# Kernel tuning notes

Hardware: AMD Instinct MI355X
Metric: run time of the kernel (lower is better)

## Reference

```python
import jax, jax.numpy as jnp
import numpy as np
from itertools import combinations

NUM_FIELDS = 40
EMB_DIM = 64
BATCH = 2048
PAIRS = NUM_FIELDS * (NUM_FIELDS - 1) // 2  # 780

def _triu_indices():
    idx = np.array(list(combinations(range(NUM_FIELDS), 2)), dtype=np.int32)  # [PAIRS, 2]
    return idx[:, 0], idx[:, 1]

def setup_inputs() -> dict:
    key = jax.random.key(0)
    k1, k2 = jax.random.split(key)
    feature_emb = jax.random.normal(k1, (BATCH, NUM_FIELDS, EMB_DIM), dtype=jnp.float32)
    # xavier_normal for [PAIRS, EMB_DIM, EMB_DIM]: fan_in = fan_out = EMB_DIM
    std = float(np.sqrt(2.0 / (EMB_DIM + EMB_DIM)))
    bilinear_W = jax.random.normal(k2, (PAIRS, EMB_DIM, EMB_DIM), dtype=jnp.float32) * std
    left_idx, right_idx = _triu_indices()
    return {
        "feature_emb": feature_emb,
        "bilinear_W": bilinear_W,
        "left_idx": jnp.asarray(left_idx),
        "right_idx": jnp.asarray(right_idx),
    }

def reference(feature_emb, bilinear_W, left_idx, right_idx):
    # field_interaction: per-pair bilinear form
    left_emb = feature_emb[:, left_idx]    # [B, PAIRS, D]
    right_emb = feature_emb[:, right_idx]  # [B, PAIRS, D]
    # (left @ W_p) * right, per pair p
    out = jnp.einsum('bpd,pde->bpe', left_emb, bilinear_W) * right_emb
    return out
```

## Files before the change

### kernel.cpp

```cpp
#include <hip/hip_runtime.h>

#define BATCH   2048
#define NFIELDS 40
#define EMB     64
#define PAIRS   780
#define BM      128
#define NTILES  (BATCH / BM)
#define NBLOCKS (PAIRS * NTILES)
#define FEMB_ELEMS (BATCH * NFIELDS * EMB)
#define W_ELEMS    (PAIRS * EMB * EMB)

typedef __attribute__((ext_vector_type(8))) short          short8;
typedef __attribute__((ext_vector_type(8))) unsigned short ushort8;
typedef __attribute__((ext_vector_type(4))) float          fvec4;

__device__ __forceinline__ unsigned short f2bf(float f) {
    unsigned int x = __float_as_uint(f);
    return (unsigned short)((x + 0x7fffu + ((x >> 16) & 1u)) >> 16);
}
__device__ __forceinline__ float bf2f(unsigned short h) {
    return __uint_as_float(((unsigned int)h) << 16);
}
struct bfpair { unsigned short h, l; };
__device__ __forceinline__ bfpair split1(float f) {
    bfpair r;
    r.h = f2bf(f);
    r.l = f2bf(f - bf2f(r.h));
    return r;
}

__global__ __launch_bounds__(256) void prep_femb(
    const float* __restrict__ femb, unsigned short* __restrict__ Fh,
    unsigned short* __restrict__ Fl)
{
    int tid  = blockIdx.x * 256 + threadIdx.x;
    int base = tid * 8;
    fvec4 a = *(const fvec4*)&femb[base];
    fvec4 b = *(const fvec4*)&femb[base + 4];
    ushort8 hi, lo;
    #pragma unroll
    for (int i = 0; i < 4; ++i) {
        bfpair s0 = split1(a[i]);
        hi[i] = s0.h; lo[i] = s0.l;
        bfpair s1 = split1(b[i]);
        hi[i + 4] = s1.h; lo[i + 4] = s1.l;
    }
    *(ushort8*)&Fh[base] = hi;
    *(ushort8*)&Fl[base] = lo;
}

__global__ __launch_bounds__(256) void prep_w(
    const float* __restrict__ W, unsigned short* __restrict__ Wh,
    unsigned short* __restrict__ Wl)
{
    __shared__ float Ws[EMB * EMB];
    int p = blockIdx.x;
    int t = threadIdx.x;
    const float* Wp = W + (size_t)p * (EMB * EMB);
    #pragma unroll
    for (int j = 0; j < 4; ++j)
        *(fvec4*)&Ws[t * 16 + j * 4] = *(const fvec4*)&Wp[t * 16 + j * 4];
    __syncthreads();

    int e  = t & 63;
    int k0 = (t >> 6) * 16;
    #pragma unroll
    for (int j = 0; j < 2; ++j) {
        int k = k0 + j * 8;
        ushort8 hi, lo;
        #pragma unroll
        for (int i = 0; i < 8; ++i) {
            bfpair s = split1(Ws[(k + i) * EMB + e]);
            hi[i] = s.h; lo[i] = s.l;
        }
        size_t dst = (size_t)p * (EMB * EMB) + e * EMB + k;
        *(ushort8*)&Wh[dst] = hi;
        *(ushort8*)&Wl[dst] = lo;
    }
}

__global__ __launch_bounds__(256, 4) void bilinear_main(
    const unsigned short* __restrict__ Fh, const unsigned short* __restrict__ Fl,
    const unsigned short* __restrict__ Wh, const unsigned short* __restrict__ Wl,
    const float* __restrict__ femb,
    const int* __restrict__ lidx, const int* __restrict__ ridx,
    float* __restrict__ out)
{
    int d  = blockIdx.x;
    int w  = (d & 7) * (NBLOCKS / 8) + (d >> 3);
    int p  = w >> 4;
    int b0 = (w & 15) * BM;

    int lp = lidx[p];
    int rp = ridx[p];
    int t  = threadIdx.x;
    int wv = t >> 6;
    int l  = t & 63;
    int r  = l & 15;
    int g  = l >> 4;

    const unsigned short* WhP = Wh + (size_t)p * (EMB * EMB);
    const unsigned short* WlP = Wl + (size_t)p * (EMB * EMB);

    fvec4 acc[2][4] = {};
    #pragma unroll
    for (int kk = 0; kk < 2; ++kk) {
        short8 Ah[4], Al[4], Bh[2], Bl[2];
        #pragma unroll
        for (int n = 0; n < 4; ++n) {
            int off = (n * 16 + r) * EMB + kk * 32 + g * 8;
            Ah[n] = *(const short8*)&WhP[off];
            Al[n] = *(const short8*)&WlP[off];
        }
        #pragma unroll
        for (int m = 0; m < 2; ++m) {
            size_t off = ((size_t)(b0 + wv * 32 + m * 16 + r) * NFIELDS + lp) * EMB
                       + kk * 32 + g * 8;
            Bh[m] = *(const short8*)&Fh[off];
            Bl[m] = *(const short8*)&Fl[off];
        }
        #pragma unroll
        for (int m = 0; m < 2; ++m)
            #pragma unroll
            for (int n = 0; n < 4; ++n) {
                acc[m][n] = __builtin_amdgcn_mfma_f32_16x16x32_bf16(Al[n], Bh[m], acc[m][n], 0, 0, 0);
                acc[m][n] = __builtin_amdgcn_mfma_f32_16x16x32_bf16(Ah[n], Bl[m], acc[m][n], 0, 0, 0);
                acc[m][n] = __builtin_amdgcn_mfma_f32_16x16x32_bf16(Ah[n], Bh[m], acc[m][n], 0, 0, 0);
            }
    }

    #pragma unroll
    for (int m = 0; m < 2; ++m) {
        int b = b0 + wv * 32 + m * 16 + r;
        const float* Rr = femb + ((size_t)b * NFIELDS + rp) * EMB;
        float*       Or = out  + ((size_t)b * PAIRS   + p)  * EMB;
        #pragma unroll
        for (int n = 0; n < 4; ++n) {
            int e0 = n * 16 + g * 4;
            fvec4 rv = *(const fvec4*)&Rr[e0];
            fvec4 o  = acc[m][n] * rv;
            *(fvec4*)&Or[e0] = o;
        }
    }
}

extern "C" void kernel_launch(void* const* d_in, const int* in_sizes, int n_in,
                              void* d_out, int out_size, void* d_ws, size_t ws_size,
                              hipStream_t stream) {
    const float* femb = (const float*)d_in[0];
    const float* W    = (const float*)d_in[1];
    const int*   lidx = (const int*)d_in[2];
    const int*   ridx = (const int*)d_in[3];
    float*       out  = (float*)d_out;

    unsigned short* Fh  = (unsigned short*)d_ws;
    unsigned short* Fl  = Fh + FEMB_ELEMS;
    unsigned short* Whg = Fl + FEMB_ELEMS;
    unsigned short* Wlg = Whg + W_ELEMS;

    prep_femb<<<FEMB_ELEMS / (256 * 8), 256, 0, stream>>>(femb, Fh, Fl);
    prep_w   <<<PAIRS, 256, 0, stream>>>(W, Whg, Wlg);
    bilinear_main<<<NBLOCKS, 256, 0, stream>>>(Fh, Fl, Whg, Wlg, femb, lidx, ridx, out);
}
```

Baseline: 591.0 us.

## Pre-pack bf16 operands into MFMA fragment layout and swap operand roles

Both prep kernels now write the hi/lo bf16 splits of the embeddings and weights directly in per-lane MFMA fragment order. The main kernel can then load each fragment with one contiguous 16-byte-per-lane access instead of strided row reads. The embedding and weight operands swap roles in the MFMA, so each lane now holds four consecutive batch rows for one output column. As a result the epilogue changes from float4 stores to scalar loads and stores. This removes scattered operand loads, but it multiplies the number of store and load instructions on the dominant output write stream.

```diff
diff --git a/kernel.cpp b/kernel.cpp
--- a/kernel.cpp
+++ b/kernel.cpp
@@ -29,24 +29,38 @@
     return r;
 }
 
+
 __global__ __launch_bounds__(256) void prep_femb(
     const float* __restrict__ femb, unsigned short* __restrict__ Fh,
     unsigned short* __restrict__ Fl)
 {
-    int tid  = blockIdx.x * 256 + threadIdx.x;
-    int base = tid * 8;
-    fvec4 a = *(const fvec4*)&femb[base];
-    fvec4 b = *(const fvec4*)&femb[base + 4];
-    ushort8 hi, lo;
+    int tid = blockIdx.x * 256 + threadIdx.x;
+    int r   = tid & 15;
+    int bf  = tid >> 4;
+    int f   = bf % NFIELDS;
+    int b4  = bf / NFIELDS;
+
+    const float* src = femb + ((size_t)(b4 * 16 + r) * NFIELDS + f) * EMB;
+    ushort8 h8[8], l8[8];
     #pragma unroll
-    for (int i = 0; i < 4; ++i) {
-        bfpair s0 = split1(a[i]);
-        hi[i] = s0.h; lo[i] = s0.l;
-        bfpair s1 = split1(b[i]);
-        hi[i + 4] = s1.h; lo[i + 4] = s1.l;
+    for (int c = 0; c < 8; ++c) {
+        fvec4 a = *(const fvec4*)&src[c * 8];
+        fvec4 b = *(const fvec4*)&src[c * 8 + 4];
+        #pragma unroll
+        for (int i = 0; i < 4; ++i) {
+            bfpair s0 = split1(a[i]); h8[c][i]     = s0.h; l8[c][i]     = s0.l;
+            bfpair s1 = split1(b[i]); h8[c][i + 4] = s1.h; l8[c][i + 4] = s1.l;
+        }
     }
-    *(ushort8*)&Fh[base] = hi;
-    *(ushort8*)&Fl[base] = lo;
+    #pragma unroll
+    for (int kk = 0; kk < 2; ++kk)
+        #pragma unroll
+        for (int g = 0; g < 4; ++g) {
+            int c = kk * 4 + g;
+            size_t dst = ((((size_t)bf * 2) + kk) * 64 + g * 16 + r) * 8;
+            *(ushort8*)&Fh[dst] = h8[c];
+            *(ushort8*)&Fl[dst] = l8[c];
+        }
 }
 
 __global__ __launch_bounds__(256) void prep_w(
@@ -62,18 +76,21 @@
         *(fvec4*)&Ws[t * 16 + j * 4] = *(const fvec4*)&Wp[t * 16 + j * 4];
     __syncthreads();
 
-    int e  = t & 63;
-    int k0 = (t >> 6) * 16;
     #pragma unroll
-    for (int j = 0; j < 2; ++j) {
-        int k = k0 + j * 8;
+    for (int half = 0; half < 2; ++half) {
+        int c  = t + half * 256;
+        int kk = c >> 8;
+        int n  = (c >> 6) & 3;
+        int l  = c & 63;
+        int r  = l & 15;
+        int g  = l >> 4;
         ushort8 hi, lo;
         #pragma unroll
         for (int i = 0; i < 8; ++i) {
-            bfpair s = split1(Ws[(k + i) * EMB + e]);
+            bfpair s = split1(Ws[(kk * 32 + g * 8 + i) * EMB + n * 16 + r]);
             hi[i] = s.h; lo[i] = s.l;
         }
-        size_t dst = (size_t)p * (EMB * EMB) + e * EMB + k;
+        size_t dst = (size_t)p * 4096 + (size_t)c * 8;
         *(ushort8*)&Wh[dst] = hi;
         *(ushort8*)&Wl[dst] = lo;
     }
@@ -89,7 +106,7 @@
     int d  = blockIdx.x;
     int w  = (d & 7) * (NBLOCKS / 8) + (d >> 3);
     int p  = w >> 4;
-    int b0 = (w & 15) * BM;
+    int bt = w & 15;
 
     int lp = lidx[p];
     int rp = ridx[p];
@@ -99,47 +116,47 @@
     int r  = l & 15;
     int g  = l >> 4;
 
-    const unsigned short* WhP = Wh + (size_t)p * (EMB * EMB);
-    const unsigned short* WlP = Wl + (size_t)p * (EMB * EMB);
-
     fvec4 acc[2][4] = {};
     #pragma unroll
     for (int kk = 0; kk < 2; ++kk) {
-        short8 Ah[4], Al[4], Bh[2], Bl[2];
+        short8 Bh[4], Bl[4];
         #pragma unroll
         for (int n = 0; n < 4; ++n) {
-            int off = (n * 16 + r) * EMB + kk * 32 + g * 8;
-            Ah[n] = *(const short8*)&WhP[off];
-            Al[n] = *(const short8*)&WlP[off];
+            size_t off = ((size_t)p * 8 + kk * 4 + n) * 512 + l * 8;
+            Bh[n] = *(const short8*)&Wh[off];
+            Bl[n] = *(const short8*)&Wl[off];
         }
+        short8 Ah[2], Al[2];
         #pragma unroll
         for (int m = 0; m < 2; ++m) {
-            size_t off = ((size_t)(b0 + wv * 32 + m * 16 + r) * NFIELDS + lp) * EMB
-                       + kk * 32 + g * 8;
-            Bh[m] = *(const short8*)&Fh[off];
-            Bl[m] = *(const short8*)&Fl[off];
+            int b4a = bt * 8 + wv * 2 + m;
+            size_t off = (((size_t)b4a * NFIELDS + lp) * 2 + kk) * 512 + l * 8;
+            Ah[m] = *(const short8*)&Fh[off];
+            Al[m] = *(const short8*)&Fl[off];
         }
         #pragma unroll
         for (int m = 0; m < 2; ++m)
             #pragma unroll
             for (int n = 0; n < 4; ++n) {
-                acc[m][n] = __builtin_amdgcn_mfma_f32_16x16x32_bf16(Al[n], Bh[m], acc[m][n], 0, 0, 0);
-                acc[m][n] = __builtin_amdgcn_mfma_f32_16x16x32_bf16(Ah[n], Bl[m], acc[m][n], 0, 0, 0);
-                acc[m][n] = __builtin_amdgcn_mfma_f32_16x16x32_bf16(Ah[n], Bh[m], acc[m][n], 0, 0, 0);
+                acc[m][n] = __builtin_amdgcn_mfma_f32_16x16x32_bf16(Al[m], Bh[n], acc[m][n], 0, 0, 0);
+                acc[m][n] = __builtin_amdgcn_mfma_f32_16x16x32_bf16(Ah[m], Bl[n], acc[m][n], 0, 0, 0);
+                acc[m][n] = __builtin_amdgcn_mfma_f32_16x16x32_bf16(Ah[m], Bh[n], acc[m][n], 0, 0, 0);
             }
     }
 
+    int b0 = bt * BM;
     #pragma unroll
     for (int m = 0; m < 2; ++m) {
-        int b = b0 + wv * 32 + m * 16 + r;
-        const float* Rr = femb + ((size_t)b * NFIELDS + rp) * EMB;
-        float*       Or = out  + ((size_t)b * PAIRS   + p)  * EMB;
+        int bb = b0 + wv * 32 + m * 16 + g * 4;
         #pragma unroll
         for (int n = 0; n < 4; ++n) {
-            int e0 = n * 16 + g * 4;
-            fvec4 rv = *(const fvec4*)&Rr[e0];
-            fvec4 o  = acc[m][n] * rv;
-            *(fvec4*)&Or[e0] = o;
+            int e = n * 16 + r;
+            #pragma unroll
+            for (int reg = 0; reg < 4; ++reg) {
+                int b = bb + reg;
+                float R = femb[((size_t)b * NFIELDS + rp) * EMB + e];
+                out[((size_t)b * PAIRS + p) * EMB + e] = acc[m][n][reg] * R;
+            }
         }
     }
 }
@@ -158,7 +175,7 @@
     unsigned short* Whg = Fl + FEMB_ELEMS;
     unsigned short* Wlg = Whg + W_ELEMS;
 
-    prep_femb<<<FEMB_ELEMS / (256 * 8), 256, 0, stream>>>(femb, Fh, Fl);
+    prep_femb<<<(BATCH / 16) * NFIELDS * 16 / 256, 256, 0, stream>>>(femb, Fh, Fl);
     prep_w   <<<PAIRS, 256, 0, stream>>>(W, Whg, Wlg);
     bilinear_main<<<NBLOCKS, 256, 0, stream>>>(Fh, Fl, Whg, Wlg, femb, lidx, ridx, out);
 }
```

Result: faster. 527.2 us (-10.8%).
